# Kernel tuning notes

Hardware: AMD Instinct MI355X
Metric: run time of the kernel (lower is better)

The kernel has to match this reference:

```python
import jax, jax.numpy as jnp
import numpy as np

NUM_HEADS = 16
HEAD_DIM = 64
CONTEXT = 128


def setup_inputs() -> dict:
    key = jax.random.key(0)
    k1, k2, k3, k4, k5 = jax.random.split(key, 5)
    B, S, H = 4, 4096, 1024
    inputs = jax.random.normal(k1, (B, S, H), dtype=jnp.float32)
    attention_mask = jnp.ones((B, S), dtype=jnp.int32)
    s = 1.0 / np.sqrt(H)
    Wq = jax.random.normal(k2, (H, H), dtype=jnp.float32) * s
    Wk = jax.random.normal(k3, (H, H), dtype=jnp.float32) * s
    Wv = jax.random.normal(k4, (H, H), dtype=jnp.float32) * s
    Wo = jax.random.normal(k5, (H, H), dtype=jnp.float32) * s
    return {"inputs": inputs, "attention_mask": attention_mask,
            "Wq": Wq, "Wk": Wk, "Wv": Wv, "Wo": Wo}


def reference(inputs, attention_mask, Wq, Wk, Wv, Wo):
    B, S, H = inputs.shape
    nH, dh = NUM_HEADS, HEAD_DIM
    C = min(CONTEXT, S)
    ctx_start = max(0, S - C)
    scale = 1.0 / np.sqrt(dh)

    # Q from all positions; K/V only from the recent context window
    q = (inputs @ Wq.T).reshape(B, S, nH, dh).transpose(0, 2, 1, 3)      # [B,nH,S,dh]
    ctx_in = inputs[:, ctx_start:, :]                                    # [B,C,H]
    k = (ctx_in @ Wk.T).reshape(B, C, nH, dh).transpose(0, 2, 1, 3)      # [B,nH,C,dh]
    v = (ctx_in @ Wv.T).reshape(B, C, nH, dh).transpose(0, 2, 1, 3)      # [B,nH,C,dh]

    scores = jnp.einsum('bhsd,bhcd->bhsc', q, k) * scale                 # [B,nH,S,C]

    # causal mask: context position <= query position; queries strictly
    # before the context window may attend to the first context token
    qpos = jnp.arange(S)
    cpos = jnp.arange(ctx_start, ctx_start + C)
    causal = cpos[None, :] <= qpos[:, None]                              # [S,C]
    before = qpos < ctx_start
    causal = causal.at[:, 0].set(causal[:, 0] | before)
    mask = causal[None, None, :, :]                                      # [1,1,S,C]

    # padding mask on context tokens
    ctx_pad = (attention_mask[:, ctx_start:ctx_start + C] != 0)          # [B,C]
    mask = mask & ctx_pad[:, None, None, :]

    scores = jnp.where(mask, scores, -jnp.inf)
    weights = jax.nn.softmax(scores, axis=-1)

    out = jnp.einsum('bhsc,bhcd->bhsd', weights, v)                      # [B,nH,S,dh]
    out = out.transpose(0, 2, 1, 3).reshape(B, S, H)
    return out @ Wo.T
```

## Files before the change

kernel.cpp:

```cpp
#include <hip/hip_runtime.h>
#include <math.h>

#define B_ 4
#define S_ 4096
#define H_ 1024
#define NH 16
#define DH 64
#define CTX 128
#define CSTART (S_ - CTX)
#define KDIM 1024

typedef __attribute__((ext_vector_type(8))) short short8;
typedef __attribute__((ext_vector_type(4))) float floatx4;
typedef unsigned short ushort_t;

__device__ inline unsigned short f2bf(float x) {
    union { float f; unsigned u; } v; v.f = x;
    unsigned r = v.u + 0x7fffu + ((v.u >> 16) & 1u);
    return (unsigned short)(r >> 16);
}

__device__ inline uint4 pack8(float4 a, float4 b) {
    union { unsigned short us[8]; uint4 u4; } p;
    p.us[0]=f2bf(a.x); p.us[1]=f2bf(a.y); p.us[2]=f2bf(a.z); p.us[3]=f2bf(a.w);
    p.us[4]=f2bf(b.x); p.us[5]=f2bf(b.y); p.us[6]=f2bf(b.z); p.us[7]=f2bf(b.w);
    return p.u4;
}

#define GLOAD_LDS16(g, l) \
    __builtin_amdgcn_global_load_lds((__attribute__((address_space(1))) const void*)(g), \
                                     (__attribute__((address_space(3))) void*)(l), 16, 0, 0)

__global__ __launch_bounds__(256) void prep(const float* __restrict__ in,
                                            const float* __restrict__ Wq, const float* __restrict__ Wk,
                                            const float* __restrict__ Wv, const float* __restrict__ Wo,
                                            ushort_t* __restrict__ Wbf, ushort_t* __restrict__ Xs) {
    int bx = blockIdx.x;
    if (bx < 2048) {
        size_t idx = (size_t)bx * 256 + threadIdx.x;
        size_t e = idx * 8;
        int wsel = (int)(e >> 20);
        size_t off = e & 1048575;
        const float* src = wsel == 0 ? Wq : wsel == 1 ? Wk : wsel == 2 ? Wv : Wo;
        const float4* s4 = (const float4*)(src + off);
        *(uint4*)(Wbf + e) = pack8(s4[0], s4[1]);
    } else {
        int idx = (bx - 2048) * 256 + threadIdx.x;
        int e = idx * 8;
        int m = e >> 10;
        int col = e & 1023;
        int b = m >> 7, i = m & 127;
        const float4* s4 = (const float4*)(in + (size_t)(b * S_ + CSTART + i) * H_ + col);
        *(uint4*)(Xs + e) = pack8(s4[0], s4[1]);
    }
}

__global__ __launch_bounds__(256) void gemm_bf16(const ushort_t* __restrict__ A,
                                                 const ushort_t* __restrict__ W,
                                                 float* __restrict__ C, int ldc) {
    __shared__ ushort_t As[64][64];
    __shared__ ushort_t Bs[64][64];
    int tid = threadIdx.x;
    int lane = tid & 63, w = tid >> 6;
    int m0 = blockIdx.y * 64, n0 = blockIdx.x * 64;
    int f0 = tid, f1 = tid + 256;
    int r0 = f0 >> 3, g0 = (f0 & 7) ^ (r0 & 7);
    int r1 = f1 >> 3, g1 = (f1 & 7) ^ (r1 & 7);
    const ushort_t* ga0 = A + (size_t)(m0 + r0) * KDIM + g0 * 8;
    const ushort_t* ga1 = A + (size_t)(m0 + r1) * KDIM + g1 * 8;
    const ushort_t* gb0 = W + (size_t)(n0 + r0) * KDIM + g0 * 8;
    const ushort_t* gb1 = W + (size_t)(n0 + r1) * KDIM + g1 * 8;
    char* la0 = (char*)As + f0 * 16;
    char* la1 = (char*)As + f1 * 16;
    char* lb0 = (char*)Bs + f0 * 16;
    char* lb1 = (char*)Bs + f1 * 16;
    int fm = lane & 15, q = lane >> 4;
    int wr = w >> 1, wc = w & 1;
    int ma0 = wr * 32, na0 = wc * 32;
    floatx4 acc[2][2] = {};
    for (int k0 = 0; k0 < KDIM; k0 += 64) {
        GLOAD_LDS16(ga0 + k0, la0);
        GLOAD_LDS16(ga1 + k0, la1);
        GLOAD_LDS16(gb0 + k0, lb0);
        GLOAD_LDS16(gb1 + k0, lb1);
        __syncthreads();
        #pragma unroll
        for (int kb = 0; kb < 2; kb++) {
            short8 af[2], bfr[2];
            #pragma unroll
            for (int t = 0; t < 2; t++) {
                int m = ma0 + t * 16 + fm;
                int pa = (kb * 4 + q) ^ (m & 7);
                af[t] = *(const short8*)&As[m][pa * 8];
                int n = na0 + t * 16 + fm;
                int pb = (kb * 4 + q) ^ (n & 7);
                bfr[t] = *(const short8*)&Bs[n][pb * 8];
            }
            #pragma unroll
            for (int i = 0; i < 2; i++)
                #pragma unroll
                for (int j = 0; j < 2; j++)
                    acc[i][j] = __builtin_amdgcn_mfma_f32_16x16x32_bf16(af[i], bfr[j], acc[i][j], 0, 0, 0);
        }
        __syncthreads();
    }
    #pragma unroll
    for (int i = 0; i < 2; i++)
        #pragma unroll
        for (int j = 0; j < 2; j++) {
            int row = m0 + ma0 + i * 16 + q * 4;
            int col = n0 + na0 + j * 16 + fm;
            #pragma unroll
            for (int t = 0; t < 4; t++)
                C[(size_t)(row + t) * ldc + col] = acc[i][j][t];
        }
}

__global__ __launch_bounds__(256) void gemm_out(const ushort_t* __restrict__ A,
                                                const ushort_t* __restrict__ W,
                                                float* __restrict__ out,
                                                float* __restrict__ rbuf) {
    __shared__ ushort_t As[64][64];
    __shared__ ushort_t Bs[64][64];
    int tid = threadIdx.x;
    int lane = tid & 63, w = tid >> 6;
    int m0 = blockIdx.y * 64, n0 = blockIdx.x * 64;
    int f0 = tid, f1 = tid + 256;
    int r0 = f0 >> 3, g0 = (f0 & 7) ^ (r0 & 7);
    int r1 = f1 >> 3, g1 = (f1 & 7) ^ (r1 & 7);
    const ushort_t* ga0 = A + (size_t)(m0 + r0) * KDIM + g0 * 8;
    const ushort_t* ga1 = A + (size_t)(m0 + r1) * KDIM + g1 * 8;
    const ushort_t* gb0 = W + (size_t)(n0 + r0) * KDIM + g0 * 8;
    const ushort_t* gb1 = W + (size_t)(n0 + r1) * KDIM + g1 * 8;
    char* la0 = (char*)As + f0 * 16;
    char* la1 = (char*)As + f1 * 16;
    char* lb0 = (char*)Bs + f0 * 16;
    char* lb1 = (char*)Bs + f1 * 16;
    int fm = lane & 15, q = lane >> 4;
    int wr = w >> 1, wc = w & 1;
    int ma0 = wr * 32, na0 = wc * 32;
    floatx4 acc[2][2] = {};
    for (int k0 = 0; k0 < KDIM; k0 += 64) {
        GLOAD_LDS16(ga0 + k0, la0);
        GLOAD_LDS16(ga1 + k0, la1);
        GLOAD_LDS16(gb0 + k0, lb0);
        GLOAD_LDS16(gb1 + k0, lb1);
        __syncthreads();
        #pragma unroll
        for (int kb = 0; kb < 2; kb++) {
            short8 af[2], bfr[2];
            #pragma unroll
            for (int t = 0; t < 2; t++) {
                int m = ma0 + t * 16 + fm;
                int pa = (kb * 4 + q) ^ (m & 7);
                af[t] = *(const short8*)&As[m][pa * 8];
                int n = na0 + t * 16 + fm;
                int pb = (kb * 4 + q) ^ (n & 7);
                bfr[t] = *(const short8*)&Bs[n][pb * 8];
            }
            #pragma unroll
            for (int i = 0; i < 2; i++)
                #pragma unroll
                for (int j = 0; j < 2; j++)
                    acc[i][j] = __builtin_amdgcn_mfma_f32_16x16x32_bf16(af[i], bfr[j], acc[i][j], 0, 0, 0);
        }
        __syncthreads();
    }
    #pragma unroll
    for (int i = 0; i < 2; i++)
        #pragma unroll
        for (int j = 0; j < 2; j++) {
            int rowg = m0 + ma0 + i * 16 + q * 4;
            int col = n0 + na0 + j * 16 + fm;
            #pragma unroll
            for (int t = 0; t < 4; t++) {
                int m = rowg + t;
                int b = m >> 7, p = m & 127;
                float val = acc[i][j][t];
                out[(size_t)(b * S_ + CSTART + p) * H_ + col] = val;
                if (p == 0) rbuf[b * H_ + col] = val;
            }
        }
}

__global__ __launch_bounds__(512) void attn(const float* __restrict__ QKV,
                                            const int* __restrict__ amask,
                                            ushort_t* __restrict__ AO) {
    __shared__ __align__(16) char smem[55296];
    ushort_t* Qs  = (ushort_t*)(smem);
    ushort_t* Ksh = (ushort_t*)(smem + 18432);
    ushort_t* Pb  = (ushort_t*)(smem);
    float*    linv = (float*)(smem + 36864);
    int*      amk  = (int*)(smem + 37376);
    ushort_t* Vt   = (ushort_t*)(smem + 37888);

    int b = blockIdx.x >> 4;
    int h = blockIdx.x & 15;
    int tid = threadIdx.x;
    {
        int r = tid >> 2, ch = tid & 3;
        size_t base = (size_t)(b * CTX + r) * 3072 + h * 64 + ch * 16;
        const float4* qp = (const float4*)(QKV + base);
        const float4* kp = (const float4*)(QKV + base + 1024);
        const float4* vp = (const float4*)(QKV + base + 2048);
        *(uint4*)(Qs  + r * 72 + ch * 16)     = pack8(qp[0], qp[1]);
        *(uint4*)(Qs  + r * 72 + ch * 16 + 8) = pack8(qp[2], qp[3]);
        *(uint4*)(Ksh + r * 72 + ch * 16)     = pack8(kp[0], kp[1]);
        *(uint4*)(Ksh + r * 72 + ch * 16 + 8) = pack8(kp[2], kp[3]);
        float vv[16];
        float4 v0 = vp[0], v1 = vp[1], v2 = vp[2], v3 = vp[3];
        vv[0]=v0.x; vv[1]=v0.y; vv[2]=v0.z; vv[3]=v0.w;
        vv[4]=v1.x; vv[5]=v1.y; vv[6]=v1.z; vv[7]=v1.w;
        vv[8]=v2.x; vv[9]=v2.y; vv[10]=v2.z; vv[11]=v2.w;
        vv[12]=v3.x; vv[13]=v3.y; vv[14]=v3.z; vv[15]=v3.w;
        #pragma unroll
        for (int i = 0; i < 16; i++)
            Vt[(ch * 16 + i) * 136 + r] = f2bf(vv[i]);
        if (tid < 128) amk[tid] = amask[b * S_ + CSTART + tid];
    }
    __syncthreads();

    int w = tid >> 6, lane = tid & 63;
    int qt = w;
    int fm = lane & 15, quad = lane >> 4;

    short8 af[2];
    #pragma unroll
    for (int kb = 0; kb < 2; kb++)
        af[kb] = *(const short8*)(Qs + (qt * 16 + fm) * 72 + kb * 32 + quad * 8);
    floatx4 acc[8] = {};
    for (int ct = 0; ct <= qt; ct++) {
        #pragma unroll
        for (int kb = 0; kb < 2; kb++) {
            short8 bfr = *(const short8*)(Ksh + (ct * 16 + fm) * 72 + kb * 32 + quad * 8);
            acc[ct] = __builtin_amdgcn_mfma_f32_16x16x32_bf16(af[kb], bfr, acc[ct], 0, 0, 0);
        }
    }
    int myamk[8];
    #pragma unroll
    for (int ct = 0; ct < 8; ct++) myamk[ct] = amk[ct * 16 + fm];
    float mx[4], ls[4];
    #pragma unroll
    for (int t = 0; t < 4; t++) {
        int row = qt * 16 + quad * 4 + t;
        float m = -INFINITY;
        #pragma unroll
        for (int ct = 0; ct < 8; ct++) {
            int col = ct * 16 + fm;
            float s = acc[ct][t] * 0.125f;
            bool valid = (ct <= qt) && (col <= row) && (myamk[ct] != 0);
            if (valid) m = fmaxf(m, s);
        }
        #pragma unroll
        for (int off = 8; off >= 1; off >>= 1) m = fmaxf(m, __shfl_xor(m, off, 64));
        float l = 0.f;
        #pragma unroll
        for (int ct = 0; ct < 8; ct++) {
            int col = ct * 16 + fm;
            float s = acc[ct][t] * 0.125f;
            bool valid = (ct <= qt) && (col <= row) && (myamk[ct] != 0);
            float p = valid ? __expf(s - m) : 0.f;
            acc[ct][t] = p;
            l += p;
        }
        #pragma unroll
        for (int off = 8; off >= 1; off >>= 1) l += __shfl_xor(l, off, 64);
        mx[t] = m; ls[t] = l;
    }
    __syncthreads();
    #pragma unroll
    for (int t = 0; t < 4; t++) {
        int row = qt * 16 + quad * 4 + t;
        #pragma unroll
        for (int ct = 0; ct < 8; ct++)
            Pb[row * 136 + ct * 16 + fm] = f2bf(acc[ct][t]);
        if (fm == 0) linv[row] = 1.f / ls[t];
    }
    int kmax = (qt >> 1) + 1;
    floatx4 oacc[4] = {};
    for (int kb = 0; kb < kmax; kb++) {
        short8 paf = *(const short8*)(Pb + (qt * 16 + fm) * 136 + kb * 32 + quad * 8);
        #pragma unroll
        for (int dt = 0; dt < 4; dt++) {
            short8 vbf = *(const short8*)(Vt + (dt * 16 + fm) * 136 + kb * 32 + quad * 8);
            oacc[dt] = __builtin_amdgcn_mfma_f32_16x16x32_bf16(paf, vbf, oacc[dt], 0, 0, 0);
        }
    }
    #pragma unroll
    for (int t = 0; t < 4; t++) {
        int row = qt * 16 + quad * 4 + t;
        float inv = linv[row];
        #pragma unroll
        for (int dt = 0; dt < 4; dt++)
            AO[(size_t)(b * CTX + row) * H_ + h * 64 + dt * 16 + fm] = f2bf(oacc[dt][t] * inv);
    }
}

__global__ __launch_bounds__(256) void write_bcast(const float* __restrict__ rbuf,
                                                   float* __restrict__ out) {
    size_t idx = (size_t)blockIdx.x * 256 + threadIdx.x;
    int b   = (int)(idx / (CSTART * 256));
    int rem = (int)(idx % (CSTART * 256));
    int p   = rem >> 8;
    int c4  = rem & 255;
    float4 v = ((const float4*)(rbuf + (size_t)b * H_))[c4];
    ((float4*)(out + (size_t)(b * S_ + p) * H_))[c4] = v;
}

extern "C" void kernel_launch(void* const* d_in, const int* in_sizes, int n_in,
                              void* d_out, int out_size, void* d_ws, size_t ws_size,
                              hipStream_t stream) {
    const float* inputs = (const float*)d_in[0];
    const int*   amask  = (const int*)d_in[1];
    const float* Wq     = (const float*)d_in[2];
    const float* Wk     = (const float*)d_in[3];
    const float* Wv     = (const float*)d_in[4];
    const float* Wo     = (const float*)d_in[5];
    float* out = (float*)d_out;

    char* ws = (char*)d_ws;
    ushort_t* Xs   = (ushort_t*)(ws);
    ushort_t* Wbf  = (ushort_t*)(ws + (1u << 20));
    float*    QKV  = (float*)(ws + (9u << 20));
    ushort_t* AObf = (ushort_t*)(ws + (15u << 20));
    float*    rbuf = (float*)(ws + (16u << 20));

    prep<<<2304, 256, 0, stream>>>(inputs, Wq, Wk, Wv, Wo, Wbf, Xs);

    dim3 gq(3072 / 64, 512 / 64);
    gemm_bf16<<<gq, 256, 0, stream>>>(Xs, Wbf, QKV, 3072);

    attn<<<64, 512, 0, stream>>>(QKV, amask, AObf);

    dim3 go(1024 / 64, 512 / 64);
    gemm_out<<<go, 256, 0, stream>>>(AObf, Wbf + (size_t)3072 * 1024, out, rbuf);

    write_bcast<<<(B_ * CSTART * 256) / 256, 256, 0, stream>>>(rbuf, out);
}
```

Before: 156.6 us.

## Double-buffer GEMM LDS tiles and emit QKV directly as bf16

Merges the two GEMM kernels into one templated kernel and adds double-buffered LDS tiles, so the global-to-LDS load for the next K slice overlaps the MFMA work on the current one, with a single barrier per iteration. The QKV projection now writes bf16 instead of fp32, which halves that intermediate's traffic and drops the fp32-to-bf16 conversion from the attention load phase. The cost is twice the LDS per block, which may lower occupancy. Rounding to bf16 happens at the same point as before, so precision is unchanged.

```diff
diff --git a/kernel.cpp b/kernel.cpp
--- a/kernel.cpp
+++ b/kernel.cpp
@@ -55,11 +55,13 @@
     }
 }
 
-__global__ __launch_bounds__(256) void gemm_bf16(const ushort_t* __restrict__ A,
-                                                 const ushort_t* __restrict__ W,
-                                                 float* __restrict__ C, int ldc) {
-    __shared__ ushort_t As[64][64];
-    __shared__ ushort_t Bs[64][64];
+template<int MODE>
+__global__ __launch_bounds__(256) void gemm_t(const ushort_t* __restrict__ A,
+                                              const ushort_t* __restrict__ W,
+                                              void* __restrict__ Cv,
+                                              float* __restrict__ rbuf, int ldc) {
+    __shared__ ushort_t As[2][4096];
+    __shared__ ushort_t Bs[2][4096];
     int tid = threadIdx.x;
     int lane = tid & 63, w = tid >> 6;
     int m0 = blockIdx.y * 64, n0 = blockIdx.x * 64;
@@ -70,20 +72,30 @@
     const ushort_t* ga1 = A + (size_t)(m0 + r1) * KDIM + g1 * 8;
     const ushort_t* gb0 = W + (size_t)(n0 + r0) * KDIM + g0 * 8;
     const ushort_t* gb1 = W + (size_t)(n0 + r1) * KDIM + g1 * 8;
-    char* la0 = (char*)As + f0 * 16;
-    char* la1 = (char*)As + f1 * 16;
-    char* lb0 = (char*)Bs + f0 * 16;
-    char* lb1 = (char*)Bs + f1 * 16;
+    char* la0[2] = { (char*)&As[0][0] + f0 * 16, (char*)&As[1][0] + f0 * 16 };
+    char* la1[2] = { (char*)&As[0][0] + f1 * 16, (char*)&As[1][0] + f1 * 16 };
+    char* lb0[2] = { (char*)&Bs[0][0] + f0 * 16, (char*)&Bs[1][0] + f0 * 16 };
+    char* lb1[2] = { (char*)&Bs[0][0] + f1 * 16, (char*)&Bs[1][0] + f1 * 16 };
     int fm = lane & 15, q = lane >> 4;
     int wr = w >> 1, wc = w & 1;
     int ma0 = wr * 32, na0 = wc * 32;
     floatx4 acc[2][2] = {};
-    for (int k0 = 0; k0 < KDIM; k0 += 64) {
-        GLOAD_LDS16(ga0 + k0, la0);
-        GLOAD_LDS16(ga1 + k0, la1);
-        GLOAD_LDS16(gb0 + k0, lb0);
-        GLOAD_LDS16(gb1 + k0, lb1);
+    GLOAD_LDS16(ga0, la0[0]);
+    GLOAD_LDS16(ga1, la1[0]);
+    GLOAD_LDS16(gb0, lb0[0]);
+    GLOAD_LDS16(gb1, lb1[0]);
+    for (int it = 0; it < KDIM / 64; it++) {
         __syncthreads();
+        int buf = it & 1;
+        if (it + 1 < KDIM / 64) {
+            int ko = (it + 1) * 64;
+            GLOAD_LDS16(ga0 + ko, la0[buf ^ 1]);
+            GLOAD_LDS16(ga1 + ko, la1[buf ^ 1]);
+            GLOAD_LDS16(gb0 + ko, lb0[buf ^ 1]);
+            GLOAD_LDS16(gb1 + ko, lb1[buf ^ 1]);
+        }
+        const ushort_t* as = &As[buf][0];
+        const ushort_t* bs = &Bs[buf][0];
         #pragma unroll
         for (int kb = 0; kb < 2; kb++) {
             short8 af[2], bfr[2];
@@ -91,10 +103,10 @@
             for (int t = 0; t < 2; t++) {
                 int m = ma0 + t * 16 + fm;
                 int pa = (kb * 4 + q) ^ (m & 7);
-                af[t] = *(const short8*)&As[m][pa * 8];
+                af[t] = *(const short8*)&as[m * 64 + pa * 8];
                 int n = na0 + t * 16 + fm;
                 int pb = (kb * 4 + q) ^ (n & 7);
-                bfr[t] = *(const short8*)&Bs[n][pb * 8];
+                bfr[t] = *(const short8*)&bs[n * 64 + pb * 8];
             }
             #pragma unroll
             for (int i = 0; i < 2; i++)
@@ -102,69 +114,6 @@
                 for (int j = 0; j < 2; j++)
                     acc[i][j] = __builtin_amdgcn_mfma_f32_16x16x32_bf16(af[i], bfr[j], acc[i][j], 0, 0, 0);
         }
-        __syncthreads();
-    }
-    #pragma unroll
-    for (int i = 0; i < 2; i++)
-        #pragma unroll
-        for (int j = 0; j < 2; j++) {
-            int row = m0 + ma0 + i * 16 + q * 4;
-            int col = n0 + na0 + j * 16 + fm;
-            #pragma unroll
-            for (int t = 0; t < 4; t++)
-                C[(size_t)(row + t) * ldc + col] = acc[i][j][t];
-        }
-}
-
-__global__ __launch_bounds__(256) void gemm_out(const ushort_t* __restrict__ A,
-                                                const ushort_t* __restrict__ W,
-                                                float* __restrict__ out,
-                                                float* __restrict__ rbuf) {
-    __shared__ ushort_t As[64][64];
-    __shared__ ushort_t Bs[64][64];
-    int tid = threadIdx.x;
-    int lane = tid & 63, w = tid >> 6;
-    int m0 = blockIdx.y * 64, n0 = blockIdx.x * 64;
-    int f0 = tid, f1 = tid + 256;
-    int r0 = f0 >> 3, g0 = (f0 & 7) ^ (r0 & 7);
-    int r1 = f1 >> 3, g1 = (f1 & 7) ^ (r1 & 7);
-    const ushort_t* ga0 = A + (size_t)(m0 + r0) * KDIM + g0 * 8;
-    const ushort_t* ga1 = A + (size_t)(m0 + r1) * KDIM + g1 * 8;
-    const ushort_t* gb0 = W + (size_t)(n0 + r0) * KDIM + g0 * 8;
-    const ushort_t* gb1 = W + (size_t)(n0 + r1) * KDIM + g1 * 8;
-    char* la0 = (char*)As + f0 * 16;
-    char* la1 = (char*)As + f1 * 16;
-    char* lb0 = (char*)Bs + f0 * 16;
-    char* lb1 = (char*)Bs + f1 * 16;
-    int fm = lane & 15, q = lane >> 4;
-    int wr = w >> 1, wc = w & 1;
-    int ma0 = wr * 32, na0 = wc * 32;
-    floatx4 acc[2][2] = {};
-    for (int k0 = 0; k0 < KDIM; k0 += 64) {
-        GLOAD_LDS16(ga0 + k0, la0);
-        GLOAD_LDS16(ga1 + k0, la1);
-        GLOAD_LDS16(gb0 + k0, lb0);
-        GLOAD_LDS16(gb1 + k0, lb1);
-        __syncthreads();
-        #pragma unroll
-        for (int kb = 0; kb < 2; kb++) {
-            short8 af[2], bfr[2];
-            #pragma unroll
-            for (int t = 0; t < 2; t++) {
-                int m = ma0 + t * 16 + fm;
-                int pa = (kb * 4 + q) ^ (m & 7);
-                af[t] = *(const short8*)&As[m][pa * 8];
-                int n = na0 + t * 16 + fm;
-                int pb = (kb * 4 + q) ^ (n & 7);
-                bfr[t] = *(const short8*)&Bs[n][pb * 8];
-            }
-            #pragma unroll
-            for (int i = 0; i < 2; i++)
-                #pragma unroll
-                for (int j = 0; j < 2; j++)
-                    acc[i][j] = __builtin_amdgcn_mfma_f32_16x16x32_bf16(af[i], bfr[j], acc[i][j], 0, 0, 0);
-        }
-        __syncthreads();
     }
     #pragma unroll
     for (int i = 0; i < 2; i++)
@@ -174,16 +123,22 @@
             int col = n0 + na0 + j * 16 + fm;
             #pragma unroll
             for (int t = 0; t < 4; t++) {
-                int m = rowg + t;
-                int b = m >> 7, p = m & 127;
                 float val = acc[i][j][t];
-                out[(size_t)(b * S_ + CSTART + p) * H_ + col] = val;
-                if (p == 0) rbuf[b * H_ + col] = val;
+                if (MODE == 0) {
+                    ((float*)Cv)[(size_t)(rowg + t) * ldc + col] = val;
+                } else if (MODE == 1) {
+                    ((ushort_t*)Cv)[(size_t)(rowg + t) * ldc + col] = f2bf(val);
+                } else {
+                    int m = rowg + t;
+                    int b = m >> 7, p = m & 127;
+                    ((float*)Cv)[(size_t)(b * S_ + CSTART + p) * H_ + col] = val;
+                    if (p == 0) rbuf[b * H_ + col] = val;
+                }
             }
         }
 }
 
-__global__ __launch_bounds__(512) void attn(const float* __restrict__ QKV,
+__global__ __launch_bounds__(512) void attn(const ushort_t* __restrict__ QKV,
                                             const int* __restrict__ amask,
                                             ushort_t* __restrict__ AO) {
     __shared__ __align__(16) char smem[55296];
@@ -199,23 +154,21 @@
     int tid = threadIdx.x;
     {
         int r = tid >> 2, ch = tid & 3;
-        size_t base = (size_t)(b * CTX + r) * 3072 + h * 64 + ch * 16;
-        const float4* qp = (const float4*)(QKV + base);
-        const float4* kp = (const float4*)(QKV + base + 1024);
-        const float4* vp = (const float4*)(QKV + base + 2048);
-        *(uint4*)(Qs  + r * 72 + ch * 16)     = pack8(qp[0], qp[1]);
-        *(uint4*)(Qs  + r * 72 + ch * 16 + 8) = pack8(qp[2], qp[3]);
-        *(uint4*)(Ksh + r * 72 + ch * 16)     = pack8(kp[0], kp[1]);
-        *(uint4*)(Ksh + r * 72 + ch * 16 + 8) = pack8(kp[2], kp[3]);
-        float vv[16];
-        float4 v0 = vp[0], v1 = vp[1], v2 = vp[2], v3 = vp[3];
-        vv[0]=v0.x; vv[1]=v0.y; vv[2]=v0.z; vv[3]=v0.w;
-        vv[4]=v1.x; vv[5]=v1.y; vv[6]=v1.z; vv[7]=v1.w;
-        vv[8]=v2.x; vv[9]=v2.y; vv[10]=v2.z; vv[11]=v2.w;
-        vv[12]=v3.x; vv[13]=v3.y; vv[14]=v3.z; vv[15]=v3.w;
+        const ushort_t* base = QKV + (size_t)(b * CTX + r) * 3072 + h * 64 + ch * 16;
+        uint4 q0 = *(const uint4*)(base);
+        uint4 q1 = *(const uint4*)(base + 8);
+        *(uint4*)(Qs + r * 72 + ch * 16)     = q0;
+        *(uint4*)(Qs + r * 72 + ch * 16 + 8) = q1;
+        uint4 k0 = *(const uint4*)(base + 1024);
+        uint4 k1 = *(const uint4*)(base + 1024 + 8);
+        *(uint4*)(Ksh + r * 72 + ch * 16)     = k0;
+        *(uint4*)(Ksh + r * 72 + ch * 16 + 8) = k1;
+        union { uint4 u4[2]; ushort_t us[16]; } vv;
+        vv.u4[0] = *(const uint4*)(base + 2048);
+        vv.u4[1] = *(const uint4*)(base + 2048 + 8);
         #pragma unroll
         for (int i = 0; i < 16; i++)
-            Vt[(ch * 16 + i) * 136 + r] = f2bf(vv[i]);
+            Vt[(ch * 16 + i) * 136 + r] = vv.us[i];
         if (tid < 128) amk[tid] = amask[b * S_ + CSTART + tid];
     }
     __syncthreads();
@@ -239,7 +192,7 @@
     int myamk[8];
     #pragma unroll
     for (int ct = 0; ct < 8; ct++) myamk[ct] = amk[ct * 16 + fm];
-    float mx[4], ls[4];
+    float ls[4];
     #pragma unroll
     for (int t = 0; t < 4; t++) {
         int row = qt * 16 + quad * 4 + t;
@@ -265,7 +218,7 @@
         }
         #pragma unroll
         for (int off = 8; off >= 1; off >>= 1) l += __shfl_xor(l, off, 64);
-        mx[t] = m; ls[t] = l;
+        ls[t] = l;
     }
     __syncthreads();
     #pragma unroll
@@ -321,19 +274,19 @@
     char* ws = (char*)d_ws;
     ushort_t* Xs   = (ushort_t*)(ws);
     ushort_t* Wbf  = (ushort_t*)(ws + (1u << 20));
-    float*    QKV  = (float*)(ws + (9u << 20));
-    ushort_t* AObf = (ushort_t*)(ws + (15u << 20));
-    float*    rbuf = (float*)(ws + (16u << 20));
+    ushort_t* QKV  = (ushort_t*)(ws + (9u << 20));
+    ushort_t* AObf = (ushort_t*)(ws + (13u << 20));
+    float*    rbuf = (float*)(ws + (14u << 20));
 
     prep<<<2304, 256, 0, stream>>>(inputs, Wq, Wk, Wv, Wo, Wbf, Xs);
 
     dim3 gq(3072 / 64, 512 / 64);
-    gemm_bf16<<<gq, 256, 0, stream>>>(Xs, Wbf, QKV, 3072);
+    gemm_t<1><<<gq, 256, 0, stream>>>(Xs, Wbf, (void*)QKV, nullptr, 3072);
 
     attn<<<64, 512, 0, stream>>>(QKV, amask, AObf);
 
     dim3 go(1024 / 64, 512 / 64);
-    gemm_out<<<go, 256, 0, stream>>>(AObf, Wbf + (size_t)3072 * 1024, out, rbuf);
+    gemm_t<2><<<go, 256, 0, stream>>>(AObf, Wbf + (size_t)3072 * 1024, (void*)out, rbuf, H_);
 
     write_bcast<<<(B_ * CSTART * 256) / 256, 256, 0, stream>>>(rbuf, out);
 }
```

Result: no change. 159.4 us (+1.8%).
